# Kernel tuning notes

Measured on AMD Instinct MI355X. Metric: run time of the kernel, lower is better.

The kernel has to match this reference:

```python
import jax, jax.numpy as jnp
import numpy as np

NUM_CLASSES = 16
ALPHA = 1.0
BETA = 1.0
GAMMA = 1.0
MARGIN = 1.0
B, D = 65536, 1024


def setup_inputs() -> dict:
    key = jax.random.key(0)
    k1, k2, k3 = jax.random.split(key, 3)
    logits = jax.random.normal(k1, (B, NUM_CLASSES), dtype=jnp.float32)
    features = jax.random.normal(k2, (B, D), dtype=jnp.float32)
    labels = jax.random.randint(k3, (B,), 0, NUM_CLASSES)
    return {"logits": logits, "labels": labels, "features": features}


def _total_loss(logits, features, labels):
    C = NUM_CLASSES
    dt = features.dtype
    # --- cross entropy (mean reduction, matches nn.CrossEntropyLoss) ---
    logp = jax.nn.log_softmax(logits, axis=-1)
    ce = -jnp.mean(jnp.take_along_axis(logp, labels[:, None], axis=1))
    # --- per-class counts / sums via single-pass segment reduce ---
    counts = jax.ops.segment_sum(jnp.ones((features.shape[0],), dt), labels, num_segments=C)  # [C]
    sums = jax.ops.segment_sum(features, labels, num_segments=C)  # [C, D]
    valid = counts > 0
    safe_counts = jnp.where(valid, counts, jnp.ones_like(counts))
    centroids = sums / safe_counts[:, None]  # [C, D]
    # --- intra-class: mean over valid classes of mean distance-to-centroid ---
    diffs = features - centroids[labels]  # [B, D]
    dists = jnp.sqrt(jnp.sum(diffs * diffs, axis=1))  # [B]
    per_class_mean_dist = jax.ops.segment_sum(dists, labels, num_segments=C) / safe_counts
    n_valid = jnp.sum(valid.astype(dt))
    intra = jnp.where(
        n_valid > 0,
        jnp.sum(jnp.where(valid, per_class_mean_dist, 0.0)) / jnp.maximum(n_valid, 1.0),
        jnp.zeros((), dt),
    )
    # --- inter-class: mean over valid (i<j) pairs of relu(margin - ||c_i - c_j||) ---
    pair_mask = (valid[:, None] & valid[None, :]) & (jnp.arange(C)[:, None] < jnp.arange(C)[None, :])
    d2 = jnp.sum((centroids[:, None, :] - centroids[None, :, :]) ** 2, axis=-1)  # [C, C]
    d2_safe = jnp.where(pair_mask, d2, jnp.ones_like(d2))  # avoid sqrt(0) on diagonal
    cdist = jnp.sqrt(d2_safe)
    inter_terms = jnp.where(pair_mask, jax.nn.relu(MARGIN - cdist), 0.0)
    n_pairs = jnp.sum(pair_mask.astype(dt))
    inter = jnp.where(
        n_pairs > 0,
        jnp.sum(inter_terms) / jnp.maximum(n_pairs, 1.0),
        jnp.zeros((), dt),
    )
    return ALPHA * ce + BETA * inter + GAMMA * intra


def reference(logits, labels, features):
    return _total_loss(logits, features, labels)
```

## Files before the change

kernel.cpp:

```cpp
#include <hip/hip_runtime.h>
#include <math.h>

#define NCLS      16
#define B_ROWS    65536
#define MARGINc   1.0f
#define CHUNK     32
#define VCPC      256
#define KMAXPC    256
#define NBLK_CS   2048
#define NBLK_DIST 2048

#define OFF_CE     0
#define OFF_CNT    32
#define OFF_OFFS   48
#define OFF_INV    64
#define OFF_CEPART 256
#define OFF_HIST   1024
#define OFF_BASES  8192
#define OFF_CENT   16384
#define OFF_ORDER  32768
#define OFF_DISTP  98304
#define OFF_PART   131072

__global__ __launch_bounds__(256) void k_ce_hist(const float* __restrict__ logits,
                                                 const int* __restrict__ labels,
                                                 float* __restrict__ ws) {
    __shared__ int hist[NCLS];
    __shared__ float cew[4];
    int tid = threadIdx.x, lane = tid & 63, w = tid >> 6;
    int b = blockIdx.x;
    if (tid < NCLS) hist[tid] = 0;
    __syncthreads();

    int row = b * 256 + tid;
    const float4* lg = (const float4*)(logits + (size_t)row * 16);
    float4 a = lg[0], b4 = lg[1], c = lg[2], d = lg[3];
    float m = fmaxf(fmaxf(fmaxf(a.x, a.y), fmaxf(a.z, a.w)),
                    fmaxf(fmaxf(b4.x, b4.y), fmaxf(b4.z, b4.w)));
    m = fmaxf(m, fmaxf(fmaxf(c.x, c.y), fmaxf(c.z, c.w)));
    m = fmaxf(m, fmaxf(fmaxf(d.x, d.y), fmaxf(d.z, d.w)));
    float s = expf(a.x - m) + expf(a.y - m) + expf(a.z - m) + expf(a.w - m)
            + expf(b4.x - m) + expf(b4.y - m) + expf(b4.z - m) + expf(b4.w - m)
            + expf(c.x - m) + expf(c.y - m) + expf(c.z - m) + expf(c.w - m)
            + expf(d.x - m) + expf(d.y - m) + expf(d.z - m) + expf(d.w - m);
    int lab = labels[row];
    atomicAdd(&hist[lab], 1);
    float xl = logits[(size_t)row * 16 + lab];
    float ce = (m + logf(s)) - xl;
    for (int o = 32; o >= 1; o >>= 1) ce += __shfl_down(ce, o, 64);
    if (lane == 0) cew[w] = ce;
    __syncthreads();
    if (tid == 0) ws[OFF_CEPART + b] = cew[0] + cew[1] + cew[2] + cew[3];
    if (tid < NCLS) ((int*)ws)[OFF_HIST + tid * 256 + b] = hist[tid];
}

__global__ __launch_bounds__(1024) void k_prefix(float* __restrict__ ws) {
    __shared__ int ctot[NCLS];
    __shared__ float cew[4];
    int tid = threadIdx.x, lane = tid & 63, w = tid >> 6;
    const int* hist = (const int*)ws + OFF_HIST;
    int* bases = (int*)ws + OFF_BASES;

    int base = lane * 4;
    int v0 = hist[w * 256 + base + 0];
    int v1 = hist[w * 256 + base + 1];
    int v2 = hist[w * 256 + base + 2];
    int v3 = hist[w * 256 + base + 3];
    int tot = v0 + v1 + v2 + v3;
    int x = tot;
    for (int o = 1; o < 64; o <<= 1) {
        int y = __shfl_up(x, o, 64);
        if (lane >= o) x += y;
    }
    int excl = x - tot;
    if (lane == 63) ctot[w] = x;
    __syncthreads();
    int off = 0;
    for (int cc = 0; cc < NCLS; ++cc) if (cc < w) off += ctot[cc];
    bases[w * 256 + base + 0] = off + excl;
    bases[w * 256 + base + 1] = off + excl + v0;
    bases[w * 256 + base + 2] = off + excl + v0 + v1;
    bases[w * 256 + base + 3] = off + excl + v0 + v1 + v2;
    if (lane == 0) {
        int cnt = ctot[w];
        ((int*)ws)[OFF_CNT + w] = cnt;
        ((int*)ws)[OFF_OFFS + w] = off;
        ws[OFF_INV + w] = 1.0f / (float)(cnt > 0 ? cnt : 1);
    }
    float s = (tid < 256) ? ws[OFF_CEPART + tid] : 0.f;
    if (tid < 256) {
        for (int o = 32; o >= 1; o >>= 1) s += __shfl_down(s, o, 64);
        if (lane == 0) cew[w] = s;
    }
    __syncthreads();
    if (tid == 0) ws[OFF_CE] = cew[0] + cew[1] + cew[2] + cew[3];
}

__global__ __launch_bounds__(256) void k_scatter(const int* __restrict__ labels,
                                                 float* __restrict__ ws) {
    __shared__ int cur[NCLS];
    int tid = threadIdx.x, b = blockIdx.x;
    if (tid < NCLS) cur[tid] = ((int*)ws)[OFF_BASES + tid * 256 + b];
    __syncthreads();
    int row = b * 256 + tid;
    int lab = labels[row];
    int pos = atomicAdd(&cur[lab], 1);
    ((int*)ws)[OFF_ORDER + pos] = row;
}

#define CADD(V) { acc.x += V.x; acc.y += V.y; acc.z += V.z; acc.w += V.w; }
__global__ __launch_bounds__(256) void k_csums(const float* __restrict__ feat,
                                               float* __restrict__ ws) {
    int tid = threadIdx.x;
    const int* cnts  = (const int*)ws + OFF_CNT;
    const int* offs  = (const int*)ws + OFF_OFFS;
    const int* order = (const int*)ws + OFF_ORDER;
    const float4* f4 = (const float4*)feat;
    float4* part4 = (float4*)(ws + OFF_PART);

    for (int vc = blockIdx.x; vc < NCLS * VCPC; vc += NBLK_CS) {
        int c = vc >> 8, k = vc & (VCPC - 1);
        int cnt = cnts[c];
        int s0 = k * CHUNK;
        if (s0 >= cnt) continue;
        int e = s0 + CHUNK; if (e > cnt) e = cnt;
        const int* ord = order + offs[c] + s0;
        int n = e - s0;

        float4 acc = make_float4(0.f, 0.f, 0.f, 0.f);
        int i = 0;
        for (; i + 8 <= n; i += 8) {
            int i0 = ord[i], i1 = ord[i + 1], i2 = ord[i + 2], i3 = ord[i + 3];
            int i4 = ord[i + 4], i5 = ord[i + 5], i6 = ord[i + 6], i7 = ord[i + 7];
            float4 v0 = f4[(size_t)i0 * 256 + tid];
            float4 v1 = f4[(size_t)i1 * 256 + tid];
            float4 v2 = f4[(size_t)i2 * 256 + tid];
            float4 v3 = f4[(size_t)i3 * 256 + tid];
            float4 v4 = f4[(size_t)i4 * 256 + tid];
            float4 v5 = f4[(size_t)i5 * 256 + tid];
            float4 v6 = f4[(size_t)i6 * 256 + tid];
            float4 v7 = f4[(size_t)i7 * 256 + tid];
            CADD(v0) CADD(v1) CADD(v2) CADD(v3)
            CADD(v4) CADD(v5) CADD(v6) CADD(v7)
        }
        for (; i < n; ++i) {
            float4 v = f4[(size_t)ord[i] * 256 + tid];
            CADD(v)
        }
        part4[(size_t)vc * 256 + tid] = acc;
    }
}

__global__ __launch_bounds__(256) void k_cent(float* __restrict__ ws) {
    int j = blockIdx.x * 256 + threadIdx.x;
    int c = j >> 10, d = j & 1023;
    int cnt = ((const int*)ws)[OFF_CNT + c];
    int kmax = (cnt + CHUNK - 1) >> 5;
    const float* part = ws + OFF_PART + (size_t)c * KMAXPC * 1024 + d;
    float s = 0.f;
    int k = 0;
    for (; k + 4 <= kmax; k += 4)
        s += part[(size_t)k * 1024] + part[(size_t)(k + 1) * 1024]
           + part[(size_t)(k + 2) * 1024] + part[(size_t)(k + 3) * 1024];
    for (; k < kmax; ++k) s += part[(size_t)k * 1024];
    ws[OFF_CENT + j] = s * ws[OFF_INV + c];
}

#define DSQ(V, C) { float dx = V.x - C.x, dy = V.y - C.y, dz = V.z - C.z, dw = V.w - C.w; \
                    accT += dx * dx + dy * dy + dz * dz + dw * dw; }
__global__ __launch_bounds__(256) void k_dist(const float* __restrict__ feat,
                                              float* __restrict__ ws) {
    __shared__ float red[4];
    int tid = threadIdx.x, lane = tid & 63, w = tid >> 6;
    const int* cnts  = (const int*)ws + OFF_CNT;
    const int* offs  = (const int*)ws + OFF_OFFS;
    const int* order = (const int*)ws + OFF_ORDER;
    const float4* f4 = (const float4*)feat;
    const float4* c4 = (const float4*)(ws + OFF_CENT);
    float* distp = ws + OFF_DISTP;

    for (int it = 0; it < (NCLS * VCPC) / NBLK_DIST; ++it) {
        int vc = (NCLS * VCPC - 1) - (blockIdx.x + it * NBLK_DIST);
        int c = vc >> 8, k = vc & (VCPC - 1);
        int cnt = cnts[c];
        int s0 = k * CHUNK;
        if (s0 >= cnt) { if (tid == 0) distp[vc] = 0.f; continue; }
        int n = cnt - s0; if (n > CHUNK) n = CHUNK;
        const int* ord = order + offs[c] + s0;

        float4 c0 = c4[c * 256 + 0 * 64 + lane];
        float4 c1 = c4[c * 256 + 1 * 64 + lane];
        float4 c2 = c4[c * 256 + 2 * 64 + lane];
        float4 c3 = c4[c * 256 + 3 * 64 + lane];

        float wsum = 0.f;
        int rbeg = w * 8;
        int rend = rbeg + 8; if (rend > n) rend = n;
        int i = rbeg;
        for (; i + 2 <= rend; i += 2) {
            int ra = ord[i], rb = ord[i + 1];
            float4 va0 = f4[(size_t)ra * 256 + 0 * 64 + lane];
            float4 va1 = f4[(size_t)ra * 256 + 1 * 64 + lane];
            float4 va2 = f4[(size_t)ra * 256 + 2 * 64 + lane];
            float4 va3 = f4[(size_t)ra * 256 + 3 * 64 + lane];
            float4 vb0 = f4[(size_t)rb * 256 + 0 * 64 + lane];
            float4 vb1 = f4[(size_t)rb * 256 + 1 * 64 + lane];
            float4 vb2 = f4[(size_t)rb * 256 + 2 * 64 + lane];
            float4 vb3 = f4[(size_t)rb * 256 + 3 * 64 + lane];
            float accT;
            accT = 0.f; DSQ(va0, c0) DSQ(va1, c1) DSQ(va2, c2) DSQ(va3, c3)
            float accA = accT;
            accT = 0.f; DSQ(vb0, c0) DSQ(vb1, c1) DSQ(vb2, c2) DSQ(vb3, c3)
            float accB = accT;
            for (int o = 32; o >= 1; o >>= 1) {
                accA += __shfl_down(accA, o, 64);
                accB += __shfl_down(accB, o, 64);
            }
            if (lane == 0) wsum += sqrtf(accA) + sqrtf(accB);
        }
        if (i < rend) {
            int ra = ord[i];
            float4 va0 = f4[(size_t)ra * 256 + 0 * 64 + lane];
            float4 va1 = f4[(size_t)ra * 256 + 1 * 64 + lane];
            float4 va2 = f4[(size_t)ra * 256 + 2 * 64 + lane];
            float4 va3 = f4[(size_t)ra * 256 + 3 * 64 + lane];
            float accT = 0.f;
            DSQ(va0, c0) DSQ(va1, c1) DSQ(va2, c2) DSQ(va3, c3)
            for (int o = 32; o >= 1; o >>= 1) accT += __shfl_down(accT, o, 64);
            if (lane == 0) wsum += sqrtf(accT);
        }
        if (lane == 0) red[w] = wsum;
        __syncthreads();
        if (tid == 0) distp[vc] = red[0] + red[1] + red[2] + red[3];
        __syncthreads();
    }
}

__global__ __launch_bounds__(256) void k_final(float* __restrict__ ws, float* __restrict__ out) {
    __shared__ float red[256];
    __shared__ float winter[4];
    __shared__ int wcnt[4];
    int tid = threadIdx.x, lane = tid & 63, w = tid >> 6;
    const int* cnts = (const int*)ws + OFF_CNT;

    int c0 = tid & 15, g = tid >> 4;
    const float* dp = ws + OFF_DISTP;
    float s = 0.f;
    for (int k = g; k < VCPC; k += 16) s += dp[(c0 << 8) + k];
    red[tid] = s;
    __syncthreads();

    const float4* c4 = (const float4*)(ws + OFF_CENT);
    float interAcc = 0.f; int pairAcc = 0;
    for (int p = w; p < 120; p += 4) {
        int i = 0, rem = p;
        while (rem >= 15 - i) { rem -= 15 - i; ++i; }
        int j = i + 1 + rem;
        int ci = cnts[i], cj = cnts[j];
        float acc = 0.f;
#pragma unroll
        for (int k = 0; k < 4; ++k) {
            float4 a = c4[i * 256 + k * 64 + lane];
            float4 b = c4[j * 256 + k * 64 + lane];
            float dx = a.x - b.x, dy = a.y - b.y, dz = a.z - b.z, dw = a.w - b.w;
            acc += dx * dx + dy * dy + dz * dz + dw * dw;
        }
        for (int o = 32; o >= 1; o >>= 1) acc += __shfl_down(acc, o, 64);
        if (lane == 0 && ci > 0 && cj > 0) {
            float t = MARGINc - sqrtf(acc);
            if (t > 0.f) interAcc += t;
            pairAcc += 1;
        }
    }
    if (lane == 0) { winter[w] = interAcc; wcnt[w] = pairAcc; }
    __syncthreads();
    if (tid == 0) {
        float interSum = winter[0] + winter[1] + winter[2] + winter[3];
        int np = wcnt[0] + wcnt[1] + wcnt[2] + wcnt[3];
        float inter = np > 0 ? interSum / (float)np : 0.f;
        float intra = 0.f; int nv = 0;
        for (int cc = 0; cc < NCLS; ++cc) {
            float dsum = 0.f;
            for (int gg = 0; gg < 16; ++gg) dsum += red[gg * 16 + cc];
            if (cnts[cc] > 0) { intra += dsum * ws[OFF_INV + cc]; nv++; }
        }
        intra = nv > 0 ? intra / (float)nv : 0.f;
        float ce = ws[OFF_CE] / (float)B_ROWS;
        out[0] = ce + inter + intra;
    }
}

extern "C" void kernel_launch(void* const* d_in, const int* in_sizes, int n_in,
                              void* d_out, int out_size, void* d_ws, size_t ws_size,
                              hipStream_t stream) {
    const float* logits = (const float*)d_in[0];
    const int* labels   = (const int*)d_in[1];
    const float* feat   = (const float*)d_in[2];
    float* ws  = (float*)d_ws;
    float* out = (float*)d_out;

    hipLaunchKernelGGL(k_ce_hist, dim3(256),       dim3(256),  0, stream, logits, labels, ws);
    hipLaunchKernelGGL(k_prefix,  dim3(1),         dim3(1024), 0, stream, ws);
    hipLaunchKernelGGL(k_scatter, dim3(256),       dim3(256),  0, stream, labels, ws);
    hipLaunchKernelGGL(k_csums,   dim3(NBLK_CS),   dim3(256),  0, stream, feat, ws);
    hipLaunchKernelGGL(k_cent,    dim3(64),        dim3(256),  0, stream, ws);
    hipLaunchKernelGGL(k_dist,    dim3(NBLK_DIST), dim3(256),  0, stream, feat, ws);
    hipLaunchKernelGGL(k_final,   dim3(1),         dim3(256),  0, stream, ws, out);
}
```

Baseline: 147.6 us.

## Fuse all stages into one cooperative persistent kernel with grid syncs

Replaces the seven-kernel pipeline with a single cooperative kernel that runs CE/histogram, prefix scan, scatter, centroid sums, centroid finalize, distance and final reduction as phases separated by grid-wide syncs. Work is regrouped into 1024 windows, with larger 128-row chunks per class so there are fewer partials to reduce. The aim is to remove per-launch gaps and the small serial kernels. The cost is six grid barriers, a fixed grid size taken from the occupancy query, and phases where only one block or 64 blocks do work. If the cooperative launch fails, it falls back to the original kernels.

After: 503.0 us. 241% more time.

```diff
diff --git a/kernel.cpp b/kernel.cpp
--- a/kernel.cpp
+++ b/kernel.cpp
@@ -1,37 +1,304 @@
 #include <hip/hip_runtime.h>
+#include <hip/hip_cooperative_groups.h>
 #include <math.h>
 
-#define NCLS      16
-#define B_ROWS    65536
-#define MARGINc   1.0f
+#define NCLS    16
+#define B_ROWS  65536
+#define MARGINc 1.0f
+#define NWIN    1024
+
+namespace cg = cooperative_groups;
+
+#define CADD(V) { acc.x += V.x; acc.y += V.y; acc.z += V.z; acc.w += V.w; }
+#define DSQ(V, C) { float dx = V.x - C.x, dy = V.y - C.y, dz = V.z - C.z, dw = V.w - C.w; \
+                    accT += dx * dx + dy * dy + dz * dz + dw * dw; }
+
+#define M_CE     0
+#define M_CNT    32
+#define M_OFFS   48
+#define M_INV    64
+#define M_CEPART 256
+#define M_HIST   2048
+#define M_BASES  32768
+#define M_CENT   65536
+#define M_ORDER  81920
+#define M_DISTP  147456
+#define M_PART   163840
+
+__global__ __launch_bounds__(256) void k_mega(const float* __restrict__ logits,
+                                              const int* __restrict__ labels,
+                                              const float* __restrict__ feat,
+                                              float* __restrict__ ws,
+                                              float* __restrict__ out) {
+    cg::grid_group gridg = cg::this_grid();
+    __shared__ int ish[NCLS];
+    __shared__ float fsh[4];
+    __shared__ float red[256];
+    __shared__ int ctot[NCLS];
+
+    const int tid = threadIdx.x, lane = tid & 63, w = tid >> 6;
+    const int b0 = blockIdx.x;
+    const int NB = gridDim.x;
+    int* wsi = (int*)ws;
+    const float4* f4 = (const float4*)feat;
+
+    for (int vb = b0; vb < NWIN; vb += NB) {
+        if (tid < NCLS) ish[tid] = 0;
+        __syncthreads();
+        int q = tid >> 2, sub = tid & 3;
+        int row = vb * 64 + q;
+        float4 lg = ((const float4*)(logits + (size_t)row * 16))[sub];
+        int lab = labels[row];
+        float m = fmaxf(fmaxf(lg.x, lg.y), fmaxf(lg.z, lg.w));
+        m = fmaxf(m, __shfl_xor(m, 1, 64));
+        m = fmaxf(m, __shfl_xor(m, 2, 64));
+        float s = expf(lg.x - m) + expf(lg.y - m) + expf(lg.z - m) + expf(lg.w - m);
+        s += __shfl_xor(s, 1, 64);
+        s += __shfl_xor(s, 2, 64);
+        float pick = 0.f;
+        if ((lab >> 2) == sub) {
+            int cmp = lab & 3;
+            pick = cmp == 0 ? lg.x : cmp == 1 ? lg.y : cmp == 2 ? lg.z : lg.w;
+        }
+        pick += __shfl_xor(pick, 1, 64);
+        pick += __shfl_xor(pick, 2, 64);
+        float ce = 0.f;
+        if (sub == 0) {
+            ce = m + logf(s) - pick;
+            atomicAdd(&ish[lab], 1);
+        }
+        for (int o = 32; o >= 1; o >>= 1) ce += __shfl_down(ce, o, 64);
+        if (lane == 0) fsh[w] = ce;
+        __syncthreads();
+        if (tid == 0) ws[M_CEPART + vb] = fsh[0] + fsh[1] + fsh[2] + fsh[3];
+        if (tid < NCLS) wsi[M_HIST + tid * 1024 + vb] = ish[tid];
+        __syncthreads();
+    }
+    gridg.sync();
+
+    if (b0 == 0) {
+        for (int ci = 0; ci < 4; ++ci) {
+            int c = w * 4 + ci;
+            int carry = 0;
+            for (int s = 0; s < 16; ++s) {
+                int v = wsi[M_HIST + c * 1024 + s * 64 + lane];
+                int x = v;
+                for (int o = 1; o < 64; o <<= 1) {
+                    int y = __shfl_up(x, o, 64);
+                    if (lane >= o) x += y;
+                }
+                wsi[M_BASES + c * 1024 + s * 64 + lane] = carry + x - v;
+                carry += __shfl(x, 63, 64);
+            }
+            if (lane == 0) ctot[c] = carry;
+        }
+        __syncthreads();
+        if (tid == 0) {
+            int off = 0;
+            for (int c = 0; c < NCLS; ++c) {
+                int cnt = ctot[c];
+                wsi[M_CNT + c] = cnt;
+                wsi[M_OFFS + c] = off;
+                ws[M_INV + c] = 1.0f / (float)(cnt > 0 ? cnt : 1);
+                off += cnt;
+            }
+        }
+        float sv = ws[M_CEPART + tid] + ws[M_CEPART + tid + 256]
+                 + ws[M_CEPART + tid + 512] + ws[M_CEPART + tid + 768];
+        for (int o = 32; o >= 1; o >>= 1) sv += __shfl_down(sv, o, 64);
+        if (lane == 0) fsh[w] = sv;
+        __syncthreads();
+        if (tid == 0) ws[M_CE] = fsh[0] + fsh[1] + fsh[2] + fsh[3];
+    }
+    gridg.sync();
+
+    for (int vb = b0; vb < NWIN; vb += NB) {
+        if (tid < NCLS) ish[tid] = wsi[M_OFFS + tid] + wsi[M_BASES + tid * 1024 + vb];
+        __syncthreads();
+        if (tid < 64) {
+            int row = vb * 64 + tid;
+            int lab = labels[row];
+            int pos = atomicAdd(&ish[lab], 1);
+            wsi[M_ORDER + pos] = row;
+        }
+        __syncthreads();
+    }
+    gridg.sync();
+
+    for (int vb = b0; vb < NWIN; vb += NB) {
+        int c = vb >> 6, q = vb & 63;
+        int cnt = wsi[M_CNT + c];
+        int s0 = q * 128;
+        int n = cnt - s0; n = n < 0 ? 0 : (n > 128 ? 128 : n);
+        const int* ord = wsi + M_ORDER + wsi[M_OFFS + c] + s0;
+        float4 acc = make_float4(0.f, 0.f, 0.f, 0.f);
+        int i = 0;
+        for (; i + 8 <= n; i += 8) {
+            int i0 = ord[i], i1 = ord[i + 1], i2 = ord[i + 2], i3 = ord[i + 3];
+            int i4 = ord[i + 4], i5 = ord[i + 5], i6 = ord[i + 6], i7 = ord[i + 7];
+            float4 v0 = f4[(size_t)i0 * 256 + tid];
+            float4 v1 = f4[(size_t)i1 * 256 + tid];
+            float4 v2 = f4[(size_t)i2 * 256 + tid];
+            float4 v3 = f4[(size_t)i3 * 256 + tid];
+            float4 v4 = f4[(size_t)i4 * 256 + tid];
+            float4 v5 = f4[(size_t)i5 * 256 + tid];
+            float4 v6 = f4[(size_t)i6 * 256 + tid];
+            float4 v7 = f4[(size_t)i7 * 256 + tid];
+            CADD(v0) CADD(v1) CADD(v2) CADD(v3)
+            CADD(v4) CADD(v5) CADD(v6) CADD(v7)
+        }
+        for (; i < n; ++i) {
+            float4 v = f4[(size_t)ord[i] * 256 + tid];
+            CADD(v)
+        }
+        ((float4*)(ws + M_PART))[vb * 256 + tid] = acc;
+    }
+    gridg.sync();
+
+    for (int vb = b0; vb < 64; vb += NB) {
+        int j = vb * 256 + tid;
+        int c = j >> 10, d = j & 1023;
+        float s = 0.f;
+#pragma unroll 8
+        for (int q = 0; q < 64; ++q) s += ws[M_PART + (size_t)(c * 64 + q) * 1024 + d];
+        ws[M_CENT + j] = s * ws[M_INV + c];
+    }
+    gridg.sync();
+
+    {
+        const float4* c4 = (const float4*)(ws + M_CENT);
+        int kit = (NWIN - 1 - b0) / NB;
+        for (int k = kit; k >= 0; --k) {
+            int vb = b0 + k * NB;
+            int c = vb >> 6, q = vb & 63;
+            int cnt = wsi[M_CNT + c];
+            int s0 = q * 128;
+            int n = cnt - s0; n = n < 0 ? 0 : (n > 128 ? 128 : n);
+            const int* ord = wsi + M_ORDER + wsi[M_OFFS + c] + s0;
+            float4 c0 = c4[c * 256 + 0 * 64 + lane];
+            float4 c1 = c4[c * 256 + 1 * 64 + lane];
+            float4 c2 = c4[c * 256 + 2 * 64 + lane];
+            float4 c3 = c4[c * 256 + 3 * 64 + lane];
+            float wsum = 0.f;
+            int rbeg = w * 32;
+            int rend = rbeg + 32; if (rend > n) rend = n;
+            int i = rend - 1;
+            for (; i >= rbeg + 1; i -= 2) {
+                int ra = ord[i], rb = ord[i - 1];
+                float4 va0 = f4[(size_t)ra * 256 + 0 * 64 + lane];
+                float4 va1 = f4[(size_t)ra * 256 + 1 * 64 + lane];
+                float4 va2 = f4[(size_t)ra * 256 + 2 * 64 + lane];
+                float4 va3 = f4[(size_t)ra * 256 + 3 * 64 + lane];
+                float4 vb0 = f4[(size_t)rb * 256 + 0 * 64 + lane];
+                float4 vb1 = f4[(size_t)rb * 256 + 1 * 64 + lane];
+                float4 vb2 = f4[(size_t)rb * 256 + 2 * 64 + lane];
+                float4 vb3 = f4[(size_t)rb * 256 + 3 * 64 + lane];
+                float accT;
+                accT = 0.f; DSQ(va0, c0) DSQ(va1, c1) DSQ(va2, c2) DSQ(va3, c3)
+                float accA = accT;
+                accT = 0.f; DSQ(vb0, c0) DSQ(vb1, c1) DSQ(vb2, c2) DSQ(vb3, c3)
+                float accB = accT;
+                for (int o = 32; o >= 1; o >>= 1) {
+                    accA += __shfl_down(accA, o, 64);
+                    accB += __shfl_down(accB, o, 64);
+                }
+                if (lane == 0) wsum += sqrtf(accA) + sqrtf(accB);
+            }
+            if (i == rbeg) {
+                int ra = ord[i];
+                float4 va0 = f4[(size_t)ra * 256 + 0 * 64 + lane];
+                float4 va1 = f4[(size_t)ra * 256 + 1 * 64 + lane];
+                float4 va2 = f4[(size_t)ra * 256 + 2 * 64 + lane];
+                float4 va3 = f4[(size_t)ra * 256 + 3 * 64 + lane];
+                float accT = 0.f;
+                DSQ(va0, c0) DSQ(va1, c1) DSQ(va2, c2) DSQ(va3, c3)
+                for (int o = 32; o >= 1; o >>= 1) accT += __shfl_down(accT, o, 64);
+                if (lane == 0) wsum += sqrtf(accT);
+            }
+            if (lane == 0) fsh[w] = wsum;
+            __syncthreads();
+            if (tid == 0) ws[M_DISTP + vb] = fsh[0] + fsh[1] + fsh[2] + fsh[3];
+            __syncthreads();
+        }
+    }
+    gridg.sync();
+
+    if (b0 == 0) {
+        const int* cnts = wsi + M_CNT;
+        int c = tid >> 4, g = tid & 15;
+        float s = ws[M_DISTP + c * 64 + g]      + ws[M_DISTP + c * 64 + g + 16]
+                + ws[M_DISTP + c * 64 + g + 32] + ws[M_DISTP + c * 64 + g + 48];
+        red[tid] = s;
+        __syncthreads();
+
+        const float4* c4 = (const float4*)(ws + M_CENT);
+        float interAcc = 0.f; int pairAcc = 0;
+        for (int p = w; p < 120; p += 4) {
+            int i = 0, rem = p;
+            while (rem >= 15 - i) { rem -= 15 - i; ++i; }
+            int j = i + 1 + rem;
+            int ci = cnts[i], cj = cnts[j];
+            float acc = 0.f;
+#pragma unroll
+            for (int k = 0; k < 4; ++k) {
+                float4 a = c4[i * 256 + k * 64 + lane];
+                float4 bb = c4[j * 256 + k * 64 + lane];
+                float dx = a.x - bb.x, dy = a.y - bb.y, dz = a.z - bb.z, dw = a.w - bb.w;
+                acc += dx * dx + dy * dy + dz * dz + dw * dw;
+            }
+            for (int o = 32; o >= 1; o >>= 1) acc += __shfl_down(acc, o, 64);
+            if (lane == 0 && ci > 0 && cj > 0) {
+                float t = MARGINc - sqrtf(acc);
+                if (t > 0.f) interAcc += t;
+                pairAcc += 1;
+            }
+        }
+        if (lane == 0) { fsh[w] = interAcc; ish[w] = pairAcc; }
+        __syncthreads();
+        if (tid == 0) {
+            float interSum = fsh[0] + fsh[1] + fsh[2] + fsh[3];
+            int np = ish[0] + ish[1] + ish[2] + ish[3];
+            float inter = np > 0 ? interSum / (float)np : 0.f;
+            float intra = 0.f; int nv = 0;
+            for (int cc = 0; cc < NCLS; ++cc) {
+                float dsum = 0.f;
+                for (int gg = 0; gg < 16; ++gg) dsum += red[cc * 16 + gg];
+                if (cnts[cc] > 0) { intra += dsum * ws[M_INV + cc]; nv++; }
+            }
+            intra = nv > 0 ? intra / (float)nv : 0.f;
+            float ce = ws[M_CE] / (float)B_ROWS;
+            out[0] = ce + inter + intra;
+        }
+    }
+}
+
 #define CHUNK     32
 #define VCPC      256
 #define KMAXPC    256
 #define NBLK_CS   2048
 #define NBLK_DIST 2048
 
-#define OFF_CE     0
-#define OFF_CNT    32
-#define OFF_OFFS   48
-#define OFF_INV    64
-#define OFF_CEPART 256
-#define OFF_HIST   1024
-#define OFF_BASES  8192
-#define OFF_CENT   16384
-#define OFF_ORDER  32768
-#define OFF_DISTP  98304
-#define OFF_PART   131072
-
-__global__ __launch_bounds__(256) void k_ce_hist(const float* __restrict__ logits,
-                                                 const int* __restrict__ labels,
-                                                 float* __restrict__ ws) {
+#define F_CE     0
+#define F_CNT    32
+#define F_OFFS   48
+#define F_INV    64
+#define F_CEPART 256
+#define F_HIST   1024
+#define F_BASES  8192
+#define F_CENT   16384
+#define F_ORDER  32768
+#define F_DISTP  98304
+#define F_PART   131072
+
+__global__ __launch_bounds__(256) void k7_ce_hist(const float* __restrict__ logits,
+                                                  const int* __restrict__ labels,
+                                                  float* __restrict__ ws) {
     __shared__ int hist[NCLS];
     __shared__ float cew[4];
     int tid = threadIdx.x, lane = tid & 63, w = tid >> 6;
     int b = blockIdx.x;
     if (tid < NCLS) hist[tid] = 0;
     __syncthreads();
-
     int row = b * 256 + tid;
     const float4* lg = (const float4*)(logits + (size_t)row * 16);
     float4 a = lg[0], b4 = lg[1], c = lg[2], d = lg[3];
@@ -50,17 +317,16 @@
     for (int o = 32; o >= 1; o >>= 1) ce += __shfl_down(ce, o, 64);
     if (lane == 0) cew[w] = ce;
     __syncthreads();
-    if (tid == 0) ws[OFF_CEPART + b] = cew[0] + cew[1] + cew[2] + cew[3];
-    if (tid < NCLS) ((int*)ws)[OFF_HIST + tid * 256 + b] = hist[tid];
-}
-
-__global__ __launch_bounds__(1024) void k_prefix(float* __restrict__ ws) {
+    if (tid == 0) ws[F_CEPART + b] = cew[0] + cew[1] + cew[2] + cew[3];
+    if (tid < NCLS) ((int*)ws)[F_HIST + tid * 256 + b] = hist[tid];
+}
+
+__global__ __launch_bounds__(1024) void k7_prefix(float* __restrict__ ws) {
     __shared__ int ctot[NCLS];
     __shared__ float cew[4];
     int tid = threadIdx.x, lane = tid & 63, w = tid >> 6;
-    const int* hist = (const int*)ws + OFF_HIST;
-    int* bases = (int*)ws + OFF_BASES;
-
+    const int* hist = (const int*)ws + F_HIST;
+    int* bases = (int*)ws + F_BASES;
     int base = lane * 4;
     int v0 = hist[w * 256 + base + 0];
     int v1 = hist[w * 256 + base + 1];
@@ -83,41 +349,39 @@
     bases[w * 256 + base + 3] = off + excl + v0 + v1 + v2;
     if (lane == 0) {
         int cnt = ctot[w];
-        ((int*)ws)[OFF_CNT + w] = cnt;
-        ((int*)ws)[OFF_OFFS + w] = off;
-        ws[OFF_INV + w] = 1.0f / (float)(cnt > 0 ? cnt : 1);
-    }
-    float s = (tid < 256) ? ws[OFF_CEPART + tid] : 0.f;
+        ((int*)ws)[F_CNT + w] = cnt;
+        ((int*)ws)[F_OFFS + w] = off;
+        ws[F_INV + w] = 1.0f / (float)(cnt > 0 ? cnt : 1);
+    }
+    float s = (tid < 256) ? ws[F_CEPART + tid] : 0.f;
     if (tid < 256) {
         for (int o = 32; o >= 1; o >>= 1) s += __shfl_down(s, o, 64);
         if (lane == 0) cew[w] = s;
     }
     __syncthreads();
-    if (tid == 0) ws[OFF_CE] = cew[0] + cew[1] + cew[2] + cew[3];
-}
-
-__global__ __launch_bounds__(256) void k_scatter(const int* __restrict__ labels,
-                                                 float* __restrict__ ws) {
+    if (tid == 0) ws[F_CE] = cew[0] + cew[1] + cew[2] + cew[3];
+}
+
+__global__ __launch_bounds__(256) void k7_scatter(const int* __restrict__ labels,
+                                                  float* __restrict__ ws) {
     __shared__ int cur[NCLS];
     int tid = threadIdx.x, b = blockIdx.x;
-    if (tid < NCLS) cur[tid] = ((int*)ws)[OFF_BASES + tid * 256 + b];
+    if (tid < NCLS) cur[tid] = ((int*)ws)[F_BASES + tid * 256 + b];
     __syncthreads();
     int row = b * 256 + tid;
     int lab = labels[row];
     int pos = atomicAdd(&cur[lab], 1);
-    ((int*)ws)[OFF_ORDER + pos] = row;
-}
-
-#define CADD(V) { acc.x += V.x; acc.y += V.y; acc.z += V.z; acc.w += V.w; }
-__global__ __launch_bounds__(256) void k_csums(const float* __restrict__ feat,
-                                               float* __restrict__ ws) {
+    ((int*)ws)[F_ORDER + pos] = row;
+}
+
+__global__ __launch_bounds__(256) void k7_csums(const float* __restrict__ feat,
+                                                float* __restrict__ ws) {
     int tid = threadIdx.x;
-    const int* cnts  = (const int*)ws + OFF_CNT;
-    const int* offs  = (const int*)ws + OFF_OFFS;
-    const int* order = (const int*)ws + OFF_ORDER;
+    const int* cnts  = (const int*)ws + F_CNT;
+    const int* offs  = (const int*)ws + F_OFFS;
+    const int* order = (const int*)ws + F_ORDER;
     const float4* f4 = (const float4*)feat;
-    float4* part4 = (float4*)(ws + OFF_PART);
-
+    float4* part4 = (float4*)(ws + F_PART);
     for (int vc = blockIdx.x; vc < NCLS * VCPC; vc += NBLK_CS) {
         int c = vc >> 8, k = vc & (VCPC - 1);
         int cnt = cnts[c];
@@ -126,7 +390,6 @@
         int e = s0 + CHUNK; if (e > cnt) e = cnt;
         const int* ord = order + offs[c] + s0;
         int n = e - s0;
-
         float4 acc = make_float4(0.f, 0.f, 0.f, 0.f);
         int i = 0;
         for (; i + 8 <= n; i += 8) {
@@ -151,34 +414,31 @@
     }
 }
 
-__global__ __launch_bounds__(256) void k_cent(float* __restrict__ ws) {
+__global__ __launch_bounds__(256) void k7_cent(float* __restrict__ ws) {
     int j = blockIdx.x * 256 + threadIdx.x;
     int c = j >> 10, d = j & 1023;
-    int cnt = ((const int*)ws)[OFF_CNT + c];
+    int cnt = ((const int*)ws)[F_CNT + c];
     int kmax = (cnt + CHUNK - 1) >> 5;
-    const float* part = ws + OFF_PART + (size_t)c * KMAXPC * 1024 + d;
+    const float* part = ws + F_PART + (size_t)c * KMAXPC * 1024 + d;
     float s = 0.f;
     int k = 0;
     for (; k + 4 <= kmax; k += 4)
         s += part[(size_t)k * 1024] + part[(size_t)(k + 1) * 1024]
            + part[(size_t)(k + 2) * 1024] + part[(size_t)(k + 3) * 1024];
     for (; k < kmax; ++k) s += part[(size_t)k * 1024];
-    ws[OFF_CENT + j] = s * ws[OFF_INV + c];
-}
-
-#define DSQ(V, C) { float dx = V.x - C.x, dy = V.y - C.y, dz = V.z - C.z, dw = V.w - C.w; \
-                    accT += dx * dx + dy * dy + dz * dz + dw * dw; }
-__global__ __launch_bounds__(256) void k_dist(const float* __restrict__ feat,
-                                              float* __restrict__ ws) {
+    ws[F_CENT + j] = s * ws[F_INV + c];
+}
+
+__global__ __launch_bounds__(256) void k7_dist(const float* __restrict__ feat,
+                                               float* __restrict__ ws) {
     __shared__ float red[4];
     int tid = threadIdx.x, lane = tid & 63, w = tid >> 6;
-    const int* cnts  = (const int*)ws + OFF_CNT;
-    const int* offs  = (const int*)ws + OFF_OFFS;
-    const int* order = (const int*)ws + OFF_ORDER;
+    const int* cnts  = (const int*)ws + F_CNT;
+    const int* offs  = (const int*)ws + F_OFFS;
+    const int* order = (const int*)ws + F_ORDER;
     const float4* f4 = (const float4*)feat;
-    const float4* c4 = (const float4*)(ws + OFF_CENT);
-    float* distp = ws + OFF_DISTP;
-
+    const float4* c4 = (const float4*)(ws + F_CENT);
+    float* distp = ws + F_DISTP;
     for (int it = 0; it < (NCLS * VCPC) / NBLK_DIST; ++it) {
         int vc = (NCLS * VCPC - 1) - (blockIdx.x + it * NBLK_DIST);
         int c = vc >> 8, k = vc & (VCPC - 1);
@@ -187,12 +447,10 @@
         if (s0 >= cnt) { if (tid == 0) distp[vc] = 0.f; continue; }
         int n = cnt - s0; if (n > CHUNK) n = CHUNK;
         const int* ord = order + offs[c] + s0;
-
         float4 c0 = c4[c * 256 + 0 * 64 + lane];
         float4 c1 = c4[c * 256 + 1 * 64 + lane];
         float4 c2 = c4[c * 256 + 2 * 64 + lane];
         float4 c3 = c4[c * 256 + 3 * 64 + lane];
-
         float wsum = 0.f;
         int rbeg = w * 8;
         int rend = rbeg + 8; if (rend > n) rend = n;
@@ -236,21 +494,19 @@
     }
 }
 
-__global__ __launch_bounds__(256) void k_final(float* __restrict__ ws, float* __restrict__ out) {
+__global__ __launch_bounds__(256) void k7_final(float* __restrict__ ws, float* __restrict__ out) {
     __shared__ float red[256];
     __shared__ float winter[4];
     __shared__ int wcnt[4];
     int tid = threadIdx.x, lane = tid & 63, w = tid >> 6;
-    const int* cnts = (const int*)ws + OFF_CNT;
-
+    const int* cnts = (const int*)ws + F_CNT;
     int c0 = tid & 15, g = tid >> 4;
-    const float* dp = ws + OFF_DISTP;
+    const float* dp = ws + F_DISTP;
     float s = 0.f;
     for (int k = g; k < VCPC; k += 16) s += dp[(c0 << 8) + k];
     red[tid] = s;
     __syncthreads();
-
-    const float4* c4 = (const float4*)(ws + OFF_CENT);
+    const float4* c4 = (const float4*)(ws + F_CENT);
     float interAcc = 0.f; int pairAcc = 0;
     for (int p = w; p < 120; p += 4) {
         int i = 0, rem = p;
@@ -282,10 +538,10 @@
         for (int cc = 0; cc < NCLS; ++cc) {
             float dsum = 0.f;
             for (int gg = 0; gg < 16; ++gg) dsum += red[gg * 16 + cc];
-            if (cnts[cc] > 0) { intra += dsum * ws[OFF_INV + cc]; nv++; }
+            if (cnts[cc] > 0) { intra += dsum * ws[F_INV + cc]; nv++; }
         }
         intra = nv > 0 ? intra / (float)nv : 0.f;
-        float ce = ws[OFF_CE] / (float)B_ROWS;
+        float ce = ws[F_CE] / (float)B_ROWS;
         out[0] = ce + inter + intra;
     }
 }
@@ -299,11 +555,28 @@
     float* ws  = (float*)d_ws;
     float* out = (float*)d_out;
 
-    hipLaunchKernelGGL(k_ce_hist, dim3(256),       dim3(256),  0, stream, logits, labels, ws);
-    hipLaunchKernelGGL(k_prefix,  dim3(1),         dim3(1024), 0, stream, ws);
-    hipLaunchKernelGGL(k_scatter, dim3(256),       dim3(256),  0, stream, labels, ws);
-    hipLaunchKernelGGL(k_csums,   dim3(NBLK_CS),   dim3(256),  0, stream, feat, ws);
-    hipLaunchKernelGGL(k_cent,    dim3(64),        dim3(256),  0, stream, ws);
-    hipLaunchKernelGGL(k_dist,    dim3(NBLK_DIST), dim3(256),  0, stream, feat, ws);
-    hipLaunchKernelGGL(k_final,   dim3(1),         dim3(256),  0, stream, ws, out);
-}
+    int dev = 0;
+    (void)hipGetDevice(&dev);
+    int nCU = 0;
+    (void)hipDeviceGetAttribute(&nCU, hipDeviceAttributeMultiprocessorCount, dev);
+    int maxB = 0;
+    (void)hipOccupancyMaxActiveBlocksPerMultiprocessor(&maxB, (const void*)k_mega, 256, 0);
+    long nb = (long)maxB * (long)nCU;
+    int NB = (int)(nb > NWIN ? NWIN : nb);
+
+    hipError_t err = hipErrorUnknown;
+    if (NB >= 1) {
+        void* args[] = {(void*)&logits, (void*)&labels, (void*)&feat, (void*)&ws, (void*)&out};
+        err = hipLaunchCooperativeKernel((const void*)k_mega, dim3(NB), dim3(256), args, 0, stream);
+    }
+    if (err != hipSuccess) {
+        (void)hipGetLastError();
+        hipLaunchKernelGGL(k7_ce_hist, dim3(256),       dim3(256),  0, stream, logits, labels, ws);
+        hipLaunchKernelGGL(k7_prefix,  dim3(1),         dim3(1024), 0, stream, ws);
+        hipLaunchKernelGGL(k7_scatter, dim3(256),       dim3(256),  0, stream, labels, ws);
+        hipLaunchKernelGGL(k7_csums,   dim3(NBLK_CS),   dim3(256),  0, stream, feat, ws);
+        hipLaunchKernelGGL(k7_cent,    dim3(64),        dim3(256),  0, stream, ws);
+        hipLaunchKernelGGL(k7_dist,    dim3(NBLK_DIST), dim3(256),  0, stream, feat, ws);
+        hipLaunchKernelGGL(k7_final,   dim3(1),         dim3(256),  0, stream, ws, out);
+    }
+}
```

## Drop single-block prefix kernel by fusing scan into scatter and CE reduce into final

Applied to the files above, without the earlier changes.

Removes the single-block k_prefix launch. Each scatter block now computes its own per-class base offsets by scanning the histogram columns. The cross-entropy partial sum moves into k_final. The CE/histogram kernel now uses 1024 blocks with four lanes per row, and the scatter kernel uses 1024 small 64-thread blocks. This cuts one serial launch and widens the early kernels, at the cost of every scatter block redundantly reading the whole 16x1024 histogram.

Result: slower. 181.7 us (+23.0%).

```diff
diff --git a/kernel.cpp b/kernel.cpp
--- a/kernel.cpp
+++ b/kernel.cpp
@@ -9,114 +9,110 @@
 #define KMAXPC    256
 #define NBLK_CS   2048
 #define NBLK_DIST 2048
-
-#define OFF_CE     0
-#define OFF_CNT    32
-#define OFF_OFFS   48
-#define OFF_INV    64
-#define OFF_CEPART 256
-#define OFF_HIST   1024
-#define OFF_BASES  8192
-#define OFF_CENT   16384
-#define OFF_ORDER  32768
-#define OFF_DISTP  98304
-#define OFF_PART   131072
+#define NWIN      1024
+
+#define W_CNT    32
+#define W_OFFS   48
+#define W_INV    64
+#define W_CEPART 256
+#define W_HIST   2048
+#define W_CENT   65536
+#define W_ORDER  81920
+#define W_DISTP  147456
+#define W_PART   163840
+
+#define CADD(V) { acc.x += V.x; acc.y += V.y; acc.z += V.z; acc.w += V.w; }
+#define DSQ(V, C) { float dx = V.x - C.x, dy = V.y - C.y, dz = V.z - C.z, dw = V.w - C.w; \
+                    accT += dx * dx + dy * dy + dz * dz + dw * dw; }
 
 __global__ __launch_bounds__(256) void k_ce_hist(const float* __restrict__ logits,
                                                  const int* __restrict__ labels,
                                                  float* __restrict__ ws) {
-    __shared__ int hist[NCLS];
-    __shared__ float cew[4];
+    __shared__ int ish[NCLS];
+    __shared__ float fsh[4];
     int tid = threadIdx.x, lane = tid & 63, w = tid >> 6;
+    int vb = blockIdx.x;
+    int* wsi = (int*)ws;
+    if (tid < NCLS) ish[tid] = 0;
+    __syncthreads();
+
+    int q = tid >> 2, sub = tid & 3;
+    int row = vb * 64 + q;
+    float4 lg = ((const float4*)(logits + (size_t)row * 16))[sub];
+    int lab = labels[row];
+    float m = fmaxf(fmaxf(lg.x, lg.y), fmaxf(lg.z, lg.w));
+    m = fmaxf(m, __shfl_xor(m, 1, 64));
+    m = fmaxf(m, __shfl_xor(m, 2, 64));
+    float s = expf(lg.x - m) + expf(lg.y - m) + expf(lg.z - m) + expf(lg.w - m);
+    s += __shfl_xor(s, 1, 64);
+    s += __shfl_xor(s, 2, 64);
+    float pick = 0.f;
+    if ((lab >> 2) == sub) {
+        int cmp = lab & 3;
+        pick = cmp == 0 ? lg.x : cmp == 1 ? lg.y : cmp == 2 ? lg.z : lg.w;
+    }
+    pick += __shfl_xor(pick, 1, 64);
+    pick += __shfl_xor(pick, 2, 64);
+    float ce = 0.f;
+    if (sub == 0) {
+        ce = m + logf(s) - pick;
+        atomicAdd(&ish[lab], 1);
+    }
+    for (int o = 32; o >= 1; o >>= 1) ce += __shfl_down(ce, o, 64);
+    if (lane == 0) fsh[w] = ce;
+    __syncthreads();
+    if (tid == 0) ws[W_CEPART + vb] = fsh[0] + fsh[1] + fsh[2] + fsh[3];
+    if (tid < NCLS) wsi[W_HIST + tid * 1024 + vb] = ish[tid];
+}
+
+__global__ __launch_bounds__(64) void k_scatter(const int* __restrict__ labels,
+                                                float* __restrict__ ws) {
+    __shared__ int cur[NCLS];
+    int lane = threadIdx.x;
     int b = blockIdx.x;
-    if (tid < NCLS) hist[tid] = 0;
-    __syncthreads();
-
-    int row = b * 256 + tid;
-    const float4* lg = (const float4*)(logits + (size_t)row * 16);
-    float4 a = lg[0], b4 = lg[1], c = lg[2], d = lg[3];
-    float m = fmaxf(fmaxf(fmaxf(a.x, a.y), fmaxf(a.z, a.w)),
-                    fmaxf(fmaxf(b4.x, b4.y), fmaxf(b4.z, b4.w)));
-    m = fmaxf(m, fmaxf(fmaxf(c.x, c.y), fmaxf(c.z, c.w)));
-    m = fmaxf(m, fmaxf(fmaxf(d.x, d.y), fmaxf(d.z, d.w)));
-    float s = expf(a.x - m) + expf(a.y - m) + expf(a.z - m) + expf(a.w - m)
-            + expf(b4.x - m) + expf(b4.y - m) + expf(b4.z - m) + expf(b4.w - m)
-            + expf(c.x - m) + expf(c.y - m) + expf(c.z - m) + expf(c.w - m)
-            + expf(d.x - m) + expf(d.y - m) + expf(d.z - m) + expf(d.w - m);
-    int lab = labels[row];
-    atomicAdd(&hist[lab], 1);
-    float xl = logits[(size_t)row * 16 + lab];
-    float ce = (m + logf(s)) - xl;
-    for (int o = 32; o >= 1; o >>= 1) ce += __shfl_down(ce, o, 64);
-    if (lane == 0) cew[w] = ce;
-    __syncthreads();
-    if (tid == 0) ws[OFF_CEPART + b] = cew[0] + cew[1] + cew[2] + cew[3];
-    if (tid < NCLS) ((int*)ws)[OFF_HIST + tid * 256 + b] = hist[tid];
-}
-
-__global__ __launch_bounds__(1024) void k_prefix(float* __restrict__ ws) {
-    __shared__ int ctot[NCLS];
-    __shared__ float cew[4];
-    int tid = threadIdx.x, lane = tid & 63, w = tid >> 6;
-    const int* hist = (const int*)ws + OFF_HIST;
-    int* bases = (int*)ws + OFF_BASES;
-
-    int base = lane * 4;
-    int v0 = hist[w * 256 + base + 0];
-    int v1 = hist[w * 256 + base + 1];
-    int v2 = hist[w * 256 + base + 2];
-    int v3 = hist[w * 256 + base + 3];
-    int tot = v0 + v1 + v2 + v3;
-    int x = tot;
-    for (int o = 1; o < 64; o <<= 1) {
-        int y = __shfl_up(x, o, 64);
-        if (lane >= o) x += y;
-    }
-    int excl = x - tot;
-    if (lane == 63) ctot[w] = x;
-    __syncthreads();
-    int off = 0;
-    for (int cc = 0; cc < NCLS; ++cc) if (cc < w) off += ctot[cc];
-    bases[w * 256 + base + 0] = off + excl;
-    bases[w * 256 + base + 1] = off + excl + v0;
-    bases[w * 256 + base + 2] = off + excl + v0 + v1;
-    bases[w * 256 + base + 3] = off + excl + v0 + v1 + v2;
-    if (lane == 0) {
-        int cnt = ctot[w];
-        ((int*)ws)[OFF_CNT + w] = cnt;
-        ((int*)ws)[OFF_OFFS + w] = off;
-        ws[OFF_INV + w] = 1.0f / (float)(cnt > 0 ? cnt : 1);
-    }
-    float s = (tid < 256) ? ws[OFF_CEPART + tid] : 0.f;
-    if (tid < 256) {
-        for (int o = 32; o >= 1; o >>= 1) s += __shfl_down(s, o, 64);
-        if (lane == 0) cew[w] = s;
-    }
-    __syncthreads();
-    if (tid == 0) ws[OFF_CE] = cew[0] + cew[1] + cew[2] + cew[3];
-}
-
-__global__ __launch_bounds__(256) void k_scatter(const int* __restrict__ labels,
-                                                 float* __restrict__ ws) {
-    __shared__ int cur[NCLS];
-    int tid = threadIdx.x, b = blockIdx.x;
-    if (tid < NCLS) cur[tid] = ((int*)ws)[OFF_BASES + tid * 256 + b];
-    __syncthreads();
-    int row = b * 256 + tid;
+    int* wsi = (int*)ws;
+    const int* hist = wsi + W_HIST;
+
+    int offacc = 0;
+#pragma unroll
+    for (int c = 0; c < NCLS; ++c) {
+        int plt = 0, pall = 0;
+        for (int j = lane; j < 1024; j += 64) {
+            int h = hist[c * 1024 + j];
+            pall += h;
+            if (j < b) plt += h;
+        }
+        for (int o = 32; o >= 1; o >>= 1) {
+            plt  += __shfl_down(plt, o, 64);
+            pall += __shfl_down(pall, o, 64);
+        }
+        int cum = __shfl(plt, 0, 64);
+        int tot = __shfl(pall, 0, 64);
+        if (lane == 0) {
+            cur[c] = offacc + cum;
+            if (b == 0) {
+                wsi[W_CNT + c] = tot;
+                wsi[W_OFFS + c] = offacc;
+                ws[W_INV + c] = 1.0f / (float)(tot > 0 ? tot : 1);
+            }
+        }
+        offacc += tot;
+    }
+    __syncthreads();
+    int row = b * 64 + lane;
     int lab = labels[row];
     int pos = atomicAdd(&cur[lab], 1);
-    ((int*)ws)[OFF_ORDER + pos] = row;
-}
-
-#define CADD(V) { acc.x += V.x; acc.y += V.y; acc.z += V.z; acc.w += V.w; }
+    wsi[W_ORDER + pos] = row;
+}
+
 __global__ __launch_bounds__(256) void k_csums(const float* __restrict__ feat,
                                                float* __restrict__ ws) {
     int tid = threadIdx.x;
-    const int* cnts  = (const int*)ws + OFF_CNT;
-    const int* offs  = (const int*)ws + OFF_OFFS;
-    const int* order = (const int*)ws + OFF_ORDER;
+    const int* cnts  = (const int*)ws + W_CNT;
+    const int* offs  = (const int*)ws + W_OFFS;
+    const int* order = (const int*)ws + W_ORDER;
     const float4* f4 = (const float4*)feat;
-    float4* part4 = (float4*)(ws + OFF_PART);
+    float4* part4 = (float4*)(ws + W_PART);
 
     for (int vc = blockIdx.x; vc < NCLS * VCPC; vc += NBLK_CS) {
         int c = vc >> 8, k = vc & (VCPC - 1);
@@ -126,7 +122,6 @@
         int e = s0 + CHUNK; if (e > cnt) e = cnt;
         const int* ord = order + offs[c] + s0;
         int n = e - s0;
-
         float4 acc = make_float4(0.f, 0.f, 0.f, 0.f);
         int i = 0;
         for (; i + 8 <= n; i += 8) {
@@ -154,30 +149,28 @@
 __global__ __launch_bounds__(256) void k_cent(float* __restrict__ ws) {
     int j = blockIdx.x * 256 + threadIdx.x;
     int c = j >> 10, d = j & 1023;
-    int cnt = ((const int*)ws)[OFF_CNT + c];
+    int cnt = ((const int*)ws)[W_CNT + c];
     int kmax = (cnt + CHUNK - 1) >> 5;
-    const float* part = ws + OFF_PART + (size_t)c * KMAXPC * 1024 + d;
+    const float* part = ws + W_PART + (size_t)c * KMAXPC * 1024 + d;
     float s = 0.f;
     int k = 0;
     for (; k + 4 <= kmax; k += 4)
         s += part[(size_t)k * 1024] + part[(size_t)(k + 1) * 1024]
            + part[(size_t)(k + 2) * 1024] + part[(size_t)(k + 3) * 1024];
     for (; k < kmax; ++k) s += part[(size_t)k * 1024];
-    ws[OFF_CENT + j] = s * ws[OFF_INV + c];
-}
-
-#define DSQ(V, C) { float dx = V.x - C.x, dy = V.y - C.y, dz = V.z - C.z, dw = V.w - C.w; \
-                    accT += dx * dx + dy * dy + dz * dz + dw * dw; }
+    ws[W_CENT + j] = s * ws[W_INV + c];
+}
+
 __global__ __launch_bounds__(256) void k_dist(const float* __restrict__ feat,
                                               float* __restrict__ ws) {
     __shared__ float red[4];
     int tid = threadIdx.x, lane = tid & 63, w = tid >> 6;
-    const int* cnts  = (const int*)ws + OFF_CNT;
-    const int* offs  = (const int*)ws + OFF_OFFS;
-    const int* order = (const int*)ws + OFF_ORDER;
+    const int* cnts  = (const int*)ws + W_CNT;
+    const int* offs  = (const int*)ws + W_OFFS;
+    const int* order = (const int*)ws + W_ORDER;
     const float4* f4 = (const float4*)feat;
-    const float4* c4 = (const float4*)(ws + OFF_CENT);
-    float* distp = ws + OFF_DISTP;
+    const float4* c4 = (const float4*)(ws + W_CENT);
+    float* distp = ws + W_DISTP;
 
     for (int it = 0; it < (NCLS * VCPC) / NBLK_DIST; ++it) {
         int vc = (NCLS * VCPC - 1) - (blockIdx.x + it * NBLK_DIST);
@@ -187,12 +180,10 @@
         if (s0 >= cnt) { if (tid == 0) distp[vc] = 0.f; continue; }
         int n = cnt - s0; if (n > CHUNK) n = CHUNK;
         const int* ord = order + offs[c] + s0;
-
         float4 c0 = c4[c * 256 + 0 * 64 + lane];
         float4 c1 = c4[c * 256 + 1 * 64 + lane];
         float4 c2 = c4[c * 256 + 2 * 64 + lane];
         float4 c3 = c4[c * 256 + 3 * 64 + lane];
-
         float wsum = 0.f;
         int rbeg = w * 8;
         int rend = rbeg + 8; if (rend > n) rend = n;
@@ -240,17 +231,23 @@
     __shared__ float red[256];
     __shared__ float winter[4];
     __shared__ int wcnt[4];
+    __shared__ float cew[4];
     int tid = threadIdx.x, lane = tid & 63, w = tid >> 6;
-    const int* cnts = (const int*)ws + OFF_CNT;
+    const int* cnts = (const int*)ws + W_CNT;
+
+    float cv = ws[W_CEPART + tid] + ws[W_CEPART + tid + 256]
+             + ws[W_CEPART + tid + 512] + ws[W_CEPART + tid + 768];
+    for (int o = 32; o >= 1; o >>= 1) cv += __shfl_down(cv, o, 64);
+    if (lane == 0) cew[w] = cv;
 
     int c0 = tid & 15, g = tid >> 4;
-    const float* dp = ws + OFF_DISTP;
+    const float* dp = ws + W_DISTP;
     float s = 0.f;
     for (int k = g; k < VCPC; k += 16) s += dp[(c0 << 8) + k];
     red[tid] = s;
     __syncthreads();
 
-    const float4* c4 = (const float4*)(ws + OFF_CENT);
+    const float4* c4 = (const float4*)(ws + W_CENT);
     float interAcc = 0.f; int pairAcc = 0;
     for (int p = w; p < 120; p += 4) {
         int i = 0, rem = p;
@@ -282,10 +279,10 @@
         for (int cc = 0; cc < NCLS; ++cc) {
             float dsum = 0.f;
             for (int gg = 0; gg < 16; ++gg) dsum += red[gg * 16 + cc];
-            if (cnts[cc] > 0) { intra += dsum * ws[OFF_INV + cc]; nv++; }
+            if (cnts[cc] > 0) { intra += dsum * ws[W_INV + cc]; nv++; }
         }
         intra = nv > 0 ? intra / (float)nv : 0.f;
-        float ce = ws[OFF_CE] / (float)B_ROWS;
+        float ce = (cew[0] + cew[1] + cew[2] + cew[3]) / (float)B_ROWS;
         out[0] = ce + inter + intra;
     }
 }
@@ -299,11 +296,10 @@
     float* ws  = (float*)d_ws;
     float* out = (float*)d_out;
 
-    hipLaunchKernelGGL(k_ce_hist, dim3(256),       dim3(256),  0, stream, logits, labels, ws);
-    hipLaunchKernelGGL(k_prefix,  dim3(1),         dim3(1024), 0, stream, ws);
-    hipLaunchKernelGGL(k_scatter, dim3(256),       dim3(256),  0, stream, labels, ws);
-    hipLaunchKernelGGL(k_csums,   dim3(NBLK_CS),   dim3(256),  0, stream, feat, ws);
-    hipLaunchKernelGGL(k_cent,    dim3(64),        dim3(256),  0, stream, ws);
-    hipLaunchKernelGGL(k_dist,    dim3(NBLK_DIST), dim3(256),  0, stream, feat, ws);
-    hipLaunchKernelGGL(k_final,   dim3(1),         dim3(256),  0, stream, ws, out);
-}
+    hipLaunchKernelGGL(k_ce_hist, dim3(NWIN),      dim3(256), 0, stream, logits, labels, ws);
+    hipLaunchKernelGGL(k_scatter, dim3(NWIN),      dim3(64),  0, stream, labels, ws);
+    hipLaunchKernelGGL(k_csums,   dim3(NBLK_CS),   dim3(256), 0, stream, feat, ws);
+    hipLaunchKernelGGL(k_cent,    dim3(64),        dim3(256), 0, stream, ws);
+    hipLaunchKernelGGL(k_dist,    dim3(NBLK_DIST), dim3(256), 0, stream, feat, ws);
+    hipLaunchKernelGGL(k_final,   dim3(1),         dim3(256), 0, stream, ws, out);
+}
```
